# Performance work log

Measured on AMD Instinct MI355X. Metric: run time of the kernel, lower is better.

## Reference

```python
import jax, jax.numpy as jnp
import numpy as np

B = 4096          # batch_size
D_EMB = 16        # per-side embedding dim (embed_to_from width = 2*D_EMB)
D_HIGH = 784      # flattened high-dim feature size
NSR = 5           # negative_sample_rate
A = 1.576943      # UMAP _a
B_PARAM = 0.8950608  # UMAP _b
REPULSION = 1.0
EPS = 1e-4
GLOBAL_LOSS = 0.5
TOTAL_STEPS = 1000
BATCH_COUNT = 500  # fixed step for deterministic alpha/beta
WARMUP = int(0.05 * TOTAL_STEPS)


def _safe_sqrt(sq):
    # sqrt with zero (not NaN) gradient at 0, matching zero-distance pairs
    safe = jnp.where(sq > 0, sq, 1.0)
    return jnp.where(sq > 0, jnp.sqrt(safe), 0.0)


def _pairwise_dist(x):
    # ||x_i - x_j|| via gram trick; avoids materializing [N,N,D]
    sq = jnp.sum(x * x, axis=1)                      # [N]
    gram = x @ x.T                                   # [N,N]
    d2 = sq[:, None] + sq[None, :] - 2.0 * gram
    return _safe_sqrt(jnp.maximum(d2, 0.0))


def _umap_ce_loss(embed_to_from, perm):
    e_to, e_from = jnp.split(embed_to_from, 2, axis=1)   # [B, D_EMB] each
    neg_to = jnp.repeat(e_to, NSR, axis=0)               # [B*NSR, D_EMB]
    repeat_neg = jnp.repeat(e_from, NSR, axis=0)
    neg_from = repeat_neg[perm]                          # shuffled negatives
    d_pos = _safe_sqrt(jnp.sum((e_to - e_from) ** 2, axis=1))
    d_neg = _safe_sqrt(jnp.sum((neg_to - neg_from) ** 2, axis=1))
    dist = jnp.concatenate([d_pos, d_neg], axis=0)       # [B*(1+NSR)]
    p_dist = 1.0 / (1.0 + A * dist ** (2.0 * B_PARAM))
    p_graph = jnp.concatenate([jnp.ones(B, p_dist.dtype), jnp.zeros(B * NSR, p_dist.dtype)])
    attraction = -p_graph * jnp.log(jnp.clip(p_dist, EPS, 1.0))
    repellant = -(1.0 - p_graph) * jnp.log(jnp.clip(1.0 - p_dist, EPS, 1.0)) * REPULSION
    return jnp.mean(attraction + repellant)


def _global_feature_loss(embed_to_from, to_x):
    e_to = embed_to_from[:, :D_EMB]
    to_x = to_x.reshape(to_x.shape[0], -1)
    high_dis = _pairwise_dist(to_x)     # [N,N]
    low_dis = _pairwise_dist(e_to)      # [N,N]
    # row-wise pearson correlation between high_dis and low_dis
    h = high_dis - jnp.mean(high_dis, axis=1, keepdims=True)
    l = low_dis - jnp.mean(low_dis, axis=1, keepdims=True)
    num = jnp.sum(h * l, axis=1)
    den = jnp.sqrt(jnp.sum(h * h, axis=1)) * jnp.sqrt(jnp.sum(l * l, axis=1))
    corr = jnp.mean(num / den)
    return -corr


def _alpha_beta():
    if BATCH_COUNT >= WARMUP:
        if BATCH_COUNT <= 0.9 * TOTAL_STEPS:
            beta = max(0.0, GLOBAL_LOSS * (1 - BATCH_COUNT / (TOTAL_STEPS - WARMUP * 4)) ** 2)
        else:
            beta = 0.0
        alpha = max(0.0, 1 - beta)
    else:
        alpha = 0.0
        beta = GLOBAL_LOSS
    return alpha, beta


def setup_inputs() -> dict:
    key = jax.random.key(0)
    k1, k2, k3 = jax.random.split(key, 3)
    embed_to_from = jax.random.normal(k1, (B, 2 * D_EMB), dtype=jnp.float32)
    placeholder = jax.random.normal(k2, (B, D_HIGH), dtype=jnp.float32)
    perm = jax.random.permutation(k3, B * NSR).astype(jnp.int32)
    return {"embed_to_from": embed_to_from, "placeholder": placeholder, "perm": perm}


def reference(embed_to_from, placeholder, perm):
    loss = _umap_ce_loss(embed_to_from, perm)
    loss_g = _global_feature_loss(embed_to_from, placeholder)
    alpha, beta = _alpha_beta()
    return alpha * loss + beta * loss_g
```

## Files before the change

### kernel.cpp

```cpp
#include <hip/hip_runtime.h>
#include <hip/hip_bf16.h>
#include <math.h>

#define NB    4096
#define DH    784
#define NSR   5
#define NNEG  (NB*NSR)
#define NTOT  (NB + NNEG)

#define A_CONST 1.576943f
#define PEXP    1.7901216f
#define EPS_C   1.0e-4f
#define ALPHA_C 0.9296875f
#define BETA_C  0.0703125f

#define NBLK  528
#define CH    262144
#define SBUF  32768

typedef __hip_bfloat16 bf16;
typedef short bf16x8 __attribute__((ext_vector_type(8)));
typedef float f32x4  __attribute__((ext_vector_type(4)));
typedef float f32x2  __attribute__((ext_vector_type(2)));
typedef long long2v __attribute__((ext_vector_type(2)));

#define WS_XF8    0
#define WS_EBF    3407872
#define WS_SQX    3670016
#define WS_SQE    3686400
#define WS_ACC5   3702784
#define WS_UPART  8945664
#define WS_CNT    8946304

__device__ __forceinline__ void gl2lds16(const void* g, void* l) {
    __builtin_amdgcn_global_load_lds(
        (const __attribute__((address_space(1))) unsigned int*)g,
        (__attribute__((address_space(3))) unsigned int*)l,
        16, 0, 0);
}

__global__ void prep_fused(const float* __restrict__ X, const float* __restrict__ emb,
                           const int* __restrict__ perm, unsigned char* __restrict__ Xf8,
                           float* __restrict__ sqx, bf16* __restrict__ Ebf,
                           float* __restrict__ sqe, float* __restrict__ upart,
                           float* __restrict__ acc5, unsigned* __restrict__ cnt) {
    if (blockIdx.x == 0 && threadIdx.x == 0) *cnt = 0u;
    if (blockIdx.x < 1024) {
        const int wave = threadIdx.x >> 6, lane = threadIdx.x & 63;
        const int row = blockIdx.x * 4 + wave;
        const float4* xr = (const float4*)(X + (size_t)row * DH);
        int* xb = (int*)Xf8;
        float s = 0.f;
        #pragma unroll
        for (int it = 0; it < 4; ++it) {
            const int idx = lane + it * 64;
            if (idx < 208) {
                const int c = idx >> 4, p = idx & 15;
                const int q = p >> 2, h = (p >> 1) & 1, w = p & 1;
                const int src = c * 16 + h * 8 + q * 2 + w;
                int pk = 0;
                if (src < 196) {
                    float4 v = xr[src];
                    s += v.x * v.x + v.y * v.y + v.z * v.z + v.w * v.w;
                    int lo = __builtin_amdgcn_cvt_pk_fp8_f32(v.x, v.y, 0, false);
                    pk = __builtin_amdgcn_cvt_pk_fp8_f32(v.z, v.w, lo, true);
                }
                xb[(size_t)c * 65536 + (size_t)row * 16 + p] = pk;
            }
        }
        #pragma unroll
        for (int off = 32; off; off >>= 1) s += __shfl_down(s, off, 64);
        if (lane == 0) sqx[row] = s;
        return;
    }
    const int ub = blockIdx.x - 1024;
    const int t = ub * 256 + threadIdx.x;
    if (t < 5 * NB) acc5[t] = 0.f;
    float val = 0.f;
    if (t < NB) {
        const float4* av = (const float4*)(emb + (size_t)t * 32);
        float4 t0 = av[0], t1 = av[1], t2 = av[2], t3 = av[3];
        float4 f0 = av[4], f1 = av[5], f2 = av[6], f3 = av[7];
        bf16* eb = Ebf + (size_t)t * 32;
        union { bf16 h[4]; ushort4 u; } cv;
        #define ST4(dst, q) cv.h[0]=__float2bfloat16(q.x); cv.h[1]=__float2bfloat16(q.y); \
                            cv.h[2]=__float2bfloat16(q.z); cv.h[3]=__float2bfloat16(q.w); \
                            *(ushort4*)(dst) = cv.u;
        ST4(eb,      t0) ST4(eb + 4,  t1) ST4(eb + 8,  t2) ST4(eb + 12, t3)
        #undef ST4
        ushort4 z = {0, 0, 0, 0};
        *(ushort4*)(eb + 16) = z; *(ushort4*)(eb + 20) = z;
        *(ushort4*)(eb + 24) = z; *(ushort4*)(eb + 28) = z;
        sqe[t] = t0.x*t0.x + t0.y*t0.y + t0.z*t0.z + t0.w*t0.w
               + t1.x*t1.x + t1.y*t1.y + t1.z*t1.z + t1.w*t1.w
               + t2.x*t2.x + t2.y*t2.y + t2.z*t2.z + t2.w*t2.w
               + t3.x*t3.x + t3.y*t3.y + t3.z*t3.z + t3.w*t3.w;
        float d2 = 0.f;
        #define D2(a, b) { float4 df = {a.x-b.x, a.y-b.y, a.z-b.z, a.w-b.w}; \
                           d2 += df.x*df.x + df.y*df.y + df.z*df.z + df.w*df.w; }
        D2(t0, f0) D2(t1, f1) D2(t2, f2) D2(t3, f3)
        #undef D2
        float d = sqrtf(d2);
        float p = 1.f / (1.f + A_CONST * powf(d, PEXP));
        val = -logf(fminf(fmaxf(p, EPS_C), 1.f));
    } else if (t < NTOT) {
        const int k = t - NB;
        const int ti = k / 5;
        const int fi = perm[k] / 5;
        const float4* at = (const float4*)(emb + (size_t)ti * 32);
        const float4* bt = (const float4*)(emb + (size_t)fi * 32 + 16);
        float d2 = 0.f;
        #pragma unroll
        for (int q = 0; q < 4; ++q) {
            float4 a = at[q], b = bt[q];
            float4 df = {a.x-b.x, a.y-b.y, a.z-b.z, a.w-b.w};
            d2 += df.x*df.x + df.y*df.y + df.z*df.z + df.w*df.w;
        }
        float d = sqrtf(d2);
        float p = 1.f / (1.f + A_CONST * powf(d, PEXP));
        val = -logf(fminf(fmaxf(1.f - p, EPS_C), 1.f));
    }
    #pragma unroll
    for (int off = 32; off; off >>= 1) val += __shfl_down(val, off, 64);
    __shared__ float ps[4];
    if ((threadIdx.x & 63) == 0) ps[threadIdx.x >> 6] = val;
    __syncthreads();
    if (threadIdx.x == 0) upart[ub] = ps[0] + ps[1] + ps[2] + ps[3];
}

__global__ __launch_bounds__(512, 4) void gram_kernel(
    const unsigned char* __restrict__ Xf8, const bf16* __restrict__ Ebf,
    const float* __restrict__ sqx, const float* __restrict__ sqe,
    float* __restrict__ acc5, const float* __restrict__ upart,
    unsigned* __restrict__ cnt, float* __restrict__ out) {
    __shared__ __align__(16) unsigned char smem[67584];
    float* sqxs = (float*)(smem + 65536);
    float* sqes = (float*)(smem + 66560);
    float* scr  = (float*)smem;

    int bi, bj;
    {
        const int k = blockIdx.x & 7;
        const int idx = blockIdx.x >> 3;
        int g = -1, r = 0;
        if (k < 6) {
            const int SG[6] = {0,0,0,1,1,2}, SH[6] = {1,2,3,2,3,3};
            if (idx < 64) { bi = SG[k]*8 + (idx>>3); bj = SH[k]*8 + (idx&7); }
            else {
                const int DG[6] = {1,0,3,1,3,3};
                const int DR[6] = {32,34,30,34,32,34};
                g = DG[k]; r = DR[k] + (idx - 64);
            }
        } else if (k == 6) {
            if (idx < 34) { g = 0; r = idx; } else { g = 1; r = idx - 34; }
        } else {
            if (idx < 36) { g = 2; r = idx; } else { g = 3; r = idx - 36; }
        }
        if (g >= 0) {
            int a = 0;
            while (r >= 8 - a) { r -= 8 - a; ++a; }
            bi = g * 8 + a; bj = g * 8 + a + r;
        }
    }
    const int i0 = bi * 128, j0 = bj * 128;

    const int tid  = threadIdx.x;
    const int wave = tid >> 6;
    const int lane = tid & 63;
    const int wy = wave >> 1, wx = wave & 1;
    const int quad = lane >> 4, l15 = lane & 15;

    f32x4 acc[2][4];
    #pragma unroll
    for (int a = 0; a < 2; ++a)
        #pragma unroll
        for (int b = 0; b < 4; ++b)
            acc[a][b] = (f32x4){0.f, 0.f, 0.f, 0.f};

    const int rA  = lane >> 2;
    const int gsb = (((lane & 3) ^ ((lane >> 3) & 3))) * 16;
    const unsigned char* gA = Xf8 + (size_t)(i0 + wave * 16 + rA) * 64 + gsb;
    const unsigned char* gB = Xf8 + (size_t)(j0 + wave * 16 + rA) * 64 + gsb;
    const unsigned char* eA = (const unsigned char*)Ebf + (size_t)(i0 + wave * 16 + rA) * 64 + gsb;
    const unsigned char* eB = (const unsigned char*)Ebf + (size_t)(j0 + wave * 16 + rA) * 64 + gsb;

    if (tid < 128) {
        sqxs[tid] = sqx[i0 + tid]; sqxs[128 + tid] = sqx[j0 + tid];
        sqes[tid] = sqe[i0 + tid]; sqes[128 + tid] = sqe[j0 + tid];
    }
    __syncthreads();

#define STAGE_X(b, s) { \
        unsigned char* d = smem + (b) * SBUF + wave * 1024; \
        gl2lds16(gA + (size_t)(2 * (s)) * CH,     d); \
        gl2lds16(gA + (size_t)(2 * (s) + 1) * CH, d + 8192); \
        gl2lds16(gB + (size_t)(2 * (s)) * CH,     d + 16384); \
        gl2lds16(gB + (size_t)(2 * (s) + 1) * CH, d + 24576); }
#define STAGE_LAST(b) { \
        unsigned char* d = smem + (b) * SBUF + wave * 1024; \
        gl2lds16(gA + (size_t)12 * CH, d); \
        gl2lds16(eA,                   d + 8192); \
        gl2lds16(gB + (size_t)12 * CH, d + 16384); \
        gl2lds16(eB,                   d + 24576); }
#define MMX(aF, bF) { \
        _Pragma("unroll") \
        for (int mi = 0; mi < 2; ++mi) { \
            _Pragma("unroll") \
            for (int ni = 0; ni < 4; ++ni) { \
                acc[mi][ni] = __builtin_amdgcn_mfma_f32_16x16x32_fp8_fp8( \
                    aF[mi][0], bF[ni][0], acc[mi][ni], 0, 0, 0); \
                acc[mi][ni] = __builtin_amdgcn_mfma_f32_16x16x32_fp8_fp8( \
                    aF[mi][1], bF[ni][1], acc[mi][ni], 0, 0, 0); \
            } \
        } }

    STAGE_X(0, 0)
    STAGE_X(1, 1)

    const int key = (l15 >> 1) & 3;
    const int boX = ((quad ^ key) << 4);
    const int aro = (wy * 32 + l15) * 64 + boX;
    const int bro = (wx * 64 + l15) * 64 + boX;

    #pragma unroll
    for (int t = 0; t < 7; ++t) {
        if (t < 6) { asm volatile("s_waitcnt vmcnt(4)" ::: "memory"); }
        else       { asm volatile("s_waitcnt vmcnt(0)" ::: "memory"); }
        __builtin_amdgcn_s_barrier();
        const unsigned char* bb = smem + (t & 1) * SBUF;
        long2v aF0[2], bF0[4];
        #pragma unroll
        for (int mi = 0; mi < 2; ++mi)
            aF0[mi] = *(const long2v*)&bb[aro + mi * 1024];
        #pragma unroll
        for (int ni = 0; ni < 4; ++ni)
            bF0[ni] = *(const long2v*)&bb[16384 + bro + ni * 1024];
        __builtin_amdgcn_s_setprio(1);
        MMX(aF0, bF0)
        __builtin_amdgcn_s_setprio(0);
        if (t < 6) {
            long2v aF1[2], bF1[4];
            #pragma unroll
            for (int mi = 0; mi < 2; ++mi)
                aF1[mi] = *(const long2v*)&bb[8192 + aro + mi * 1024];
            #pragma unroll
            for (int ni = 0; ni < 4; ++ni)
                bF1[ni] = *(const long2v*)&bb[24576 + bro + ni * 1024];
            if (t < 5) {
                asm volatile("s_waitcnt lgkmcnt(0)" ::: "memory");
                __builtin_amdgcn_sched_barrier(0);
                __builtin_amdgcn_s_barrier();
                if (t < 4) { STAGE_X(t & 1, t + 2) }
                else       { STAGE_LAST(0) }
            }
            __builtin_amdgcn_s_setprio(1);
            MMX(aF1, bF1)
            __builtin_amdgcn_s_setprio(0);
        }
    }
#undef STAGE_X
#undef STAGE_LAST
#undef MMX

    bf16x8 afE[2], bfrE[4];
    #pragma unroll
    for (int mi = 0; mi < 2; ++mi)
        afE[mi] = *(const bf16x8*)&smem[8192 + aro + mi * 1024];
    #pragma unroll
    for (int ni = 0; ni < 4; ++ni)
        bfrE[ni] = *(const bf16x8*)&smem[24576 + bro + ni * 1024];
    float sqxj[4], sqej[4];
    #pragma unroll
    for (int ni = 0; ni < 4; ++ni) {
        const int jl = wx * 64 + ni * 16 + l15;
        sqxj[ni] = sqxs[128 + jl]; sqej[ni] = sqes[128 + jl];
    }
    __syncthreads();

    float cst[4][5];
    #pragma unroll
    for (int ni = 0; ni < 4; ++ni)
        #pragma unroll
        for (int c = 0; c < 5; ++c) cst[ni][c] = 0.f;

    #pragma unroll
    for (int mi = 0; mi < 2; ++mi) {
        f32x4 aE[4];
        #pragma unroll
        for (int ni = 0; ni < 4; ++ni) {
            f32x4 z = (f32x4){0.f, 0.f, 0.f, 0.f};
            aE[ni] = __builtin_amdgcn_mfma_f32_16x16x32_bf16(afE[mi], bfrE[ni], z, 0, 0, 0);
        }
        const int ilb = wy * 32 + mi * 16 + quad * 4;
        float sqxi[4], sqei[4];
        #pragma unroll
        for (int r = 0; r < 4; ++r) { sqxi[r] = sqxs[ilb + r]; sqei[r] = sqes[ilb + r]; }
        float rs[5][4];
        #pragma unroll
        for (int c = 0; c < 5; ++c)
            #pragma unroll
            for (int r = 0; r < 4; ++r) rs[c][r] = 0.f;
        #pragma unroll
        for (int ni = 0; ni < 4; ++ni) {
            const int j = j0 + wx * 64 + ni * 16 + l15;
            #pragma unroll
            for (int r = 0; r < 4; ++r) {
                const int i = i0 + ilb + r;
                float H, L;
                if (i == j) { H = 0.f; L = 0.f; }
                else {
                    float d2  = sqxi[r] + sqxj[ni] - 2.0f * acc[mi][ni][r];
                    H = sqrtf(fmaxf(d2, 0.f));
                    float d2e = sqei[r] + sqej[ni] - 2.0f * aE[ni][r];
                    L = sqrtf(fmaxf(d2e, 0.f));
                }
                rs[0][r] += H; rs[1][r] += H * H; rs[2][r] += L;
                rs[3][r] += L * L; rs[4][r] += H * L;
                cst[ni][0] += H; cst[ni][1] += H * H; cst[ni][2] += L;
                cst[ni][3] += L * L; cst[ni][4] += H * L;
            }
        }
        #pragma unroll
        for (int c = 0; c < 5; ++c)
            #pragma unroll
            for (int r = 0; r < 4; ++r)
                scr[(size_t)((((wx * 5 + c) << 6) + (wy << 4) + (quad << 2) + r)) * 18 + l15]
                    = rs[c][r];
        __syncthreads();
        for (int o = tid; o < 320; o += 512) {
            const int c = o >> 6, li = o & 63;
            const float* p0 = scr + (size_t)((c << 6) + li) * 18;
            const float* p1 = scr + (size_t)(((5 + c) << 6) + li) * 18;
            float s = 0.f;
            #pragma unroll
            for (int k = 0; k < 16; k += 2) {
                f32x2 v0 = *(const f32x2*)&p0[k]; s += v0.x + v0.y;
                f32x2 v1 = *(const f32x2*)&p1[k]; s += v1.x + v1.y;
            }
            const int iloc = ((li >> 4) << 5) + mi * 16 + (li & 15);
            unsafeAtomicAdd(&acc5[(size_t)c * NB + (i0 + iloc)], s);
        }
        __syncthreads();
    }

    if (bi != bj) {
        #pragma unroll
        for (int ni = 0; ni < 4; ++ni) {
            const int jl = wx * 64 + ni * 16 + l15;
            #pragma unroll
            for (int c = 0; c < 5; ++c)
                scr[(size_t)(c * 128 + jl) * 17 + (wy << 2) + quad] = cst[ni][c];
        }
        __syncthreads();
        for (int o = tid; o < 640; o += 512) {
            const int c = o >> 7, j = o & 127;
            const float* p = scr + (size_t)(c * 128 + j) * 17;
            float s = (((p[0] + p[1]) + (p[2] + p[3])) + ((p[4] + p[5]) + (p[6] + p[7])))
                    + (((p[8] + p[9]) + (p[10] + p[11])) + ((p[12] + p[13]) + (p[14] + p[15])));
            unsafeAtomicAdd(&acc5[(size_t)c * NB + (j0 + j)], s);
        }
    }

    __shared__ int lastFlag;
    __syncthreads();
    if (tid == 0) {
        __threadfence();
        lastFlag = (atomicAdd(cnt, 1u) == (unsigned)(NBLK - 1));
    }
    __syncthreads();
    if (lastFlag) {
        __threadfence();
        const float invN = 1.0f / (float)NB;
        float v = 0.f;
        #pragma unroll
        for (int rr = 0; rr < 8; ++rr) {
            const int r = tid + rr * 512;
            const float a  = acc5[0 * NB + r];
            const float b  = acc5[1 * NB + r];
            const float c2 = acc5[2 * NB + r];
            const float d  = acc5[3 * NB + r];
            const float e  = acc5[4 * NB + r];
            float num = e - a * c2 * invN;
            float vh  = fmaxf(b - a * a * invN, 0.f);
            float vl  = fmaxf(d - c2 * c2 * invN, 0.f);
            v += num / (sqrtf(vh) * sqrtf(vl));
        }
        v *= (-BETA_C * invN);
        if (tid < 96) v += upart[tid] * (ALPHA_C / (float)NTOT);
        #pragma unroll
        for (int off = 32; off; off >>= 1) v += __shfl_down(v, off, 64);
        float* fin = (float*)smem;
        __syncthreads();
        if ((tid & 63) == 0) fin[tid >> 6] = v;
        __syncthreads();
        if (tid == 0)
            out[0] = ((fin[0] + fin[1]) + (fin[2] + fin[3]))
                   + ((fin[4] + fin[5]) + (fin[6] + fin[7]));
    }
}

extern "C" void kernel_launch(void* const* d_in, const int* in_sizes, int n_in,
                              void* d_out, int out_size, void* d_ws, size_t ws_size,
                              hipStream_t stream) {
    const float* emb  = (const float*)d_in[0];
    const float* ph   = (const float*)d_in[1];
    const int*   perm = (const int*)d_in[2];
    float* out = (float*)d_out;

    char* ws = (char*)d_ws;
    unsigned char* Xf8 = (unsigned char*)(ws + WS_XF8);
    bf16*  Ebf    = (bf16*) (ws + WS_EBF);
    float* sqx    = (float*)(ws + WS_SQX);
    float* sqe    = (float*)(ws + WS_SQE);
    float* acc5   = (float*)(ws + WS_ACC5);
    float* upart  = (float*)(ws + WS_UPART);
    unsigned* cnt = (unsigned*)(ws + WS_CNT);

    prep_fused<<<1120, 256, 0, stream>>>(ph, emb, perm, Xf8, sqx, Ebf, sqe, upart, acc5, cnt);
    gram_kernel<<<NBLK, 512, 0, stream>>>(Xf8, Ebf, sqx, sqe, acc5, upart, cnt, out);
}
```

Baseline: 107.7 us.

## Compute two column tiles per block to reuse A-tile loads in gram kernel

After: 122.1 us. +13.4%, slower.

```diff
diff --git a/kernel.cpp b/kernel.cpp
--- a/kernel.cpp
+++ b/kernel.cpp
@@ -14,9 +14,9 @@
 #define ALPHA_C 0.9296875f
 #define BETA_C  0.0703125f
 
-#define NBLK  528
+#define NBLK  272
 #define CH    262144
-#define SBUF  32768
+#define SBUF  24576
 
 typedef __hip_bfloat16 bf16;
 typedef short bf16x8 __attribute__((ext_vector_type(8)));
@@ -128,41 +128,24 @@
     if (threadIdx.x == 0) upart[ub] = ps[0] + ps[1] + ps[2] + ps[3];
 }
 
-__global__ __launch_bounds__(512, 4) void gram_kernel(
+__global__ __launch_bounds__(512) void gram_kernel(
     const unsigned char* __restrict__ Xf8, const bf16* __restrict__ Ebf,
     const float* __restrict__ sqx, const float* __restrict__ sqe,
     float* __restrict__ acc5, const float* __restrict__ upart,
     unsigned* __restrict__ cnt, float* __restrict__ out) {
-    __shared__ __align__(16) unsigned char smem[67584];
-    float* sqxs = (float*)(smem + 65536);
-    float* sqes = (float*)(smem + 66560);
-    float* scr  = (float*)smem;
-
-    int bi, bj;
-    {
-        const int k = blockIdx.x & 7;
-        const int idx = blockIdx.x >> 3;
-        int g = -1, r = 0;
-        if (k < 6) {
-            const int SG[6] = {0,0,0,1,1,2}, SH[6] = {1,2,3,2,3,3};
-            if (idx < 64) { bi = SG[k]*8 + (idx>>3); bj = SH[k]*8 + (idx&7); }
-            else {
-                const int DG[6] = {1,0,3,1,3,3};
-                const int DR[6] = {32,34,30,34,32,34};
-                g = DG[k]; r = DR[k] + (idx - 64);
-            }
-        } else if (k == 6) {
-            if (idx < 34) { g = 0; r = idx; } else { g = 1; r = idx - 34; }
-        } else {
-            if (idx < 36) { g = 2; r = idx; } else { g = 3; r = idx - 36; }
-        }
-        if (g >= 0) {
-            int a = 0;
-            while (r >= 8 - a) { r -= 8 - a; ++a; }
-            bi = g * 8 + a; bj = g * 8 + a + r;
-        }
-    }
-    const int i0 = bi * 128, j0 = bj * 128;
+    __shared__ __align__(16) unsigned char smem[52224];
+    float* sqxs  = (float*)(smem + 49152);
+    float* sqes  = (float*)(smem + 49664);
+    float* sqxsj = (float*)(smem + 50176);
+    float* sqesj = (float*)(smem + 51200);
+    float* scr   = (float*)smem;
+
+    int n = (blockIdx.x & 7) * 34 + (blockIdx.x >> 3);
+    int bi = 0;
+    while (n >= ((33 - bi) >> 1)) { n -= (33 - bi) >> 1; ++bi; }
+    const int bj = bi + 2 * n;
+    const int has2 = (bj < 31);
+    const int i0 = bi * 128, j0s = bj * 128;
 
     const int tid  = threadIdx.x;
     const int wave = tid >> 6;
@@ -170,47 +153,38 @@
     const int wy = wave >> 1, wx = wave & 1;
     const int quad = lane >> 4, l15 = lane & 15;
 
-    f32x4 acc[2][4];
-    #pragma unroll
-    for (int a = 0; a < 2; ++a)
-        #pragma unroll
-        for (int b = 0; b < 4; ++b)
-            acc[a][b] = (f32x4){0.f, 0.f, 0.f, 0.f};
+    f32x4 acc[2][2][4];
+    #pragma unroll
+    for (int cc = 0; cc < 2; ++cc)
+        #pragma unroll
+        for (int a = 0; a < 2; ++a)
+            #pragma unroll
+            for (int b = 0; b < 4; ++b)
+                acc[cc][a][b] = (f32x4){0.f, 0.f, 0.f, 0.f};
 
     const int rA  = lane >> 2;
     const int gsb = (((lane & 3) ^ ((lane >> 3) & 3))) * 16;
-    const unsigned char* gA = Xf8 + (size_t)(i0 + wave * 16 + rA) * 64 + gsb;
-    const unsigned char* gB = Xf8 + (size_t)(j0 + wave * 16 + rA) * 64 + gsb;
-    const unsigned char* eA = (const unsigned char*)Ebf + (size_t)(i0 + wave * 16 + rA) * 64 + gsb;
-    const unsigned char* eB = (const unsigned char*)Ebf + (size_t)(j0 + wave * 16 + rA) * 64 + gsb;
-
-    if (tid < 128) {
-        sqxs[tid] = sqx[i0 + tid]; sqxs[128 + tid] = sqx[j0 + tid];
-        sqes[tid] = sqe[i0 + tid]; sqes[128 + tid] = sqe[j0 + tid];
-    }
+    const unsigned char* gA  = Xf8 + (size_t)(i0 + wave * 16 + rA) * 64 + gsb;
+    const unsigned char* gB0 = Xf8 + (size_t)(j0s + wave * 32 + rA) * 64 + gsb;
+
+    if (tid < 128) { sqxs[tid] = sqx[i0 + tid]; sqes[tid] = sqe[i0 + tid]; }
+    if (tid < 256) { sqxsj[tid] = sqx[j0s + tid]; sqesj[tid] = sqe[j0s + tid]; }
     __syncthreads();
 
 #define STAGE_X(b, s) { \
-        unsigned char* d = smem + (b) * SBUF + wave * 1024; \
-        gl2lds16(gA + (size_t)(2 * (s)) * CH,     d); \
-        gl2lds16(gA + (size_t)(2 * (s) + 1) * CH, d + 8192); \
-        gl2lds16(gB + (size_t)(2 * (s)) * CH,     d + 16384); \
-        gl2lds16(gB + (size_t)(2 * (s) + 1) * CH, d + 24576); }
-#define STAGE_LAST(b) { \
-        unsigned char* d = smem + (b) * SBUF + wave * 1024; \
-        gl2lds16(gA + (size_t)12 * CH, d); \
-        gl2lds16(eA,                   d + 8192); \
-        gl2lds16(gB + (size_t)12 * CH, d + 16384); \
-        gl2lds16(eB,                   d + 24576); }
-#define MMX(aF, bF) { \
+        unsigned char* d = smem + (b) * SBUF; \
+        gl2lds16(gA  + (size_t)(s) * CH, d + wave * 1024); \
+        gl2lds16(gB0 + (size_t)(s) * CH, d + 8192 + wave * 2048); \
+        gl2lds16(gB0 + (size_t)(s) * CH + 1024, d + 8192 + wave * 2048 + 1024); }
+#define MMX(ac, aF, bF) { \
         _Pragma("unroll") \
         for (int mi = 0; mi < 2; ++mi) { \
             _Pragma("unroll") \
             for (int ni = 0; ni < 4; ++ni) { \
-                acc[mi][ni] = __builtin_amdgcn_mfma_f32_16x16x32_fp8_fp8( \
-                    aF[mi][0], bF[ni][0], acc[mi][ni], 0, 0, 0); \
-                acc[mi][ni] = __builtin_amdgcn_mfma_f32_16x16x32_fp8_fp8( \
-                    aF[mi][1], bF[ni][1], acc[mi][ni], 0, 0, 0); \
+                ac[mi][ni] = __builtin_amdgcn_mfma_f32_16x16x32_fp8_fp8( \
+                    aF[mi][0], bF[ni][0], ac[mi][ni], 0, 0, 0); \
+                ac[mi][ni] = __builtin_amdgcn_mfma_f32_16x16x32_fp8_fp8( \
+                    aF[mi][1], bF[ni][1], ac[mi][ni], 0, 0, 0); \
             } \
         } }
 
@@ -223,141 +197,139 @@
     const int bro = (wx * 64 + l15) * 64 + boX;
 
     #pragma unroll
-    for (int t = 0; t < 7; ++t) {
-        if (t < 6) { asm volatile("s_waitcnt vmcnt(4)" ::: "memory"); }
-        else       { asm volatile("s_waitcnt vmcnt(0)" ::: "memory"); }
+    for (int t = 0; t < 13; ++t) {
+        if (t < 12) { asm volatile("s_waitcnt vmcnt(3)" ::: "memory"); }
+        else        { asm volatile("s_waitcnt vmcnt(0)" ::: "memory"); }
         __builtin_amdgcn_s_barrier();
         const unsigned char* bb = smem + (t & 1) * SBUF;
-        long2v aF0[2], bF0[4];
+        long2v aF[2], bF0[4], bF1[4];
         #pragma unroll
         for (int mi = 0; mi < 2; ++mi)
-            aF0[mi] = *(const long2v*)&bb[aro + mi * 1024];
+            aF[mi] = *(const long2v*)&bb[aro + mi * 1024];
         #pragma unroll
         for (int ni = 0; ni < 4; ++ni)
-            bF0[ni] = *(const long2v*)&bb[16384 + bro + ni * 1024];
-        __builtin_amdgcn_s_setprio(1);
-        MMX(aF0, bF0)
-        __builtin_amdgcn_s_setprio(0);
-        if (t < 6) {
-            long2v aF1[2], bF1[4];
-            #pragma unroll
-            for (int mi = 0; mi < 2; ++mi)
-                aF1[mi] = *(const long2v*)&bb[8192 + aro + mi * 1024];
-            #pragma unroll
-            for (int ni = 0; ni < 4; ++ni)
-                bF1[ni] = *(const long2v*)&bb[24576 + bro + ni * 1024];
-            if (t < 5) {
-                asm volatile("s_waitcnt lgkmcnt(0)" ::: "memory");
-                __builtin_amdgcn_sched_barrier(0);
-                __builtin_amdgcn_s_barrier();
-                if (t < 4) { STAGE_X(t & 1, t + 2) }
-                else       { STAGE_LAST(0) }
-            }
-            __builtin_amdgcn_s_setprio(1);
-            MMX(aF1, bF1)
-            __builtin_amdgcn_s_setprio(0);
-        }
+            bF0[ni] = *(const long2v*)&bb[8192 + bro + ni * 1024];
+        #pragma unroll
+        for (int ni = 0; ni < 4; ++ni)
+            bF1[ni] = *(const long2v*)&bb[16384 + bro + ni * 1024];
+        if (t < 11) {
+            asm volatile("s_waitcnt lgkmcnt(0)" ::: "memory");
+            __builtin_amdgcn_sched_barrier(0);
+            __builtin_amdgcn_s_barrier();
+            STAGE_X(t & 1, t + 2)
+        }
+        MMX(acc[0], aF, bF0)
+        MMX(acc[1], aF, bF1)
     }
 #undef STAGE_X
-#undef STAGE_LAST
 #undef MMX
 
-    bf16x8 afE[2], bfrE[4];
+    __syncthreads();
+
+    const unsigned char* Eb = (const unsigned char*)Ebf;
+    bf16x8 afE[2];
     #pragma unroll
     for (int mi = 0; mi < 2; ++mi)
-        afE[mi] = *(const bf16x8*)&smem[8192 + aro + mi * 1024];
-    #pragma unroll
-    for (int ni = 0; ni < 4; ++ni)
-        bfrE[ni] = *(const bf16x8*)&smem[24576 + bro + ni * 1024];
-    float sqxj[4], sqej[4];
-    #pragma unroll
-    for (int ni = 0; ni < 4; ++ni) {
-        const int jl = wx * 64 + ni * 16 + l15;
-        sqxj[ni] = sqxs[128 + jl]; sqej[ni] = sqes[128 + jl];
-    }
-    __syncthreads();
-
-    float cst[4][5];
-    #pragma unroll
-    for (int ni = 0; ni < 4; ++ni)
-        #pragma unroll
-        for (int c = 0; c < 5; ++c) cst[ni][c] = 0.f;
-
-    #pragma unroll
-    for (int mi = 0; mi < 2; ++mi) {
-        f32x4 aE[4];
+        afE[mi] = *(const bf16x8*)(Eb + (size_t)(i0 + wy * 32 + mi * 16 + l15) * 64 + quad * 16);
+
+    #pragma unroll
+    for (int cc = 0; cc < 2; ++cc) {
+        if (cc == 1 && !has2) continue;
+        const int bjc = bj + cc;
+        const int j0 = bjc * 128;
+        bf16x8 bfrE[4];
+        #pragma unroll
+        for (int ni = 0; ni < 4; ++ni)
+            bfrE[ni] = *(const bf16x8*)(Eb + (size_t)(j0 + wx * 64 + ni * 16 + l15) * 64 + quad * 16);
+        float sqxj[4], sqej[4];
         #pragma unroll
         for (int ni = 0; ni < 4; ++ni) {
-            f32x4 z = (f32x4){0.f, 0.f, 0.f, 0.f};
-            aE[ni] = __builtin_amdgcn_mfma_f32_16x16x32_bf16(afE[mi], bfrE[ni], z, 0, 0, 0);
-        }
-        const int ilb = wy * 32 + mi * 16 + quad * 4;
-        float sqxi[4], sqei[4];
-        #pragma unroll
-        for (int r = 0; r < 4; ++r) { sqxi[r] = sqxs[ilb + r]; sqei[r] = sqes[ilb + r]; }
-        float rs[5][4];
-        #pragma unroll
-        for (int c = 0; c < 5; ++c)
-            #pragma unroll
-            for (int r = 0; r < 4; ++r) rs[c][r] = 0.f;
-        #pragma unroll
-        for (int ni = 0; ni < 4; ++ni) {
-            const int j = j0 + wx * 64 + ni * 16 + l15;
-            #pragma unroll
-            for (int r = 0; r < 4; ++r) {
-                const int i = i0 + ilb + r;
-                float H, L;
-                if (i == j) { H = 0.f; L = 0.f; }
-                else {
-                    float d2  = sqxi[r] + sqxj[ni] - 2.0f * acc[mi][ni][r];
-                    H = sqrtf(fmaxf(d2, 0.f));
-                    float d2e = sqei[r] + sqej[ni] - 2.0f * aE[ni][r];
-                    L = sqrtf(fmaxf(d2e, 0.f));
+            const int jl = cc * 128 + wx * 64 + ni * 16 + l15;
+            sqxj[ni] = sqxsj[jl]; sqej[ni] = sqesj[jl];
+        }
+        float cst[4][5];
+        #pragma unroll
+        for (int ni = 0; ni < 4; ++ni)
+            #pragma unroll
+            for (int c = 0; c < 5; ++c) cst[ni][c] = 0.f;
+
+        #pragma unroll
+        for (int mi = 0; mi < 2; ++mi) {
+            f32x4 aE[4];
+            #pragma unroll
+            for (int ni = 0; ni < 4; ++ni) {
+                f32x4 z = (f32x4){0.f, 0.f, 0.f, 0.f};
+                aE[ni] = __builtin_amdgcn_mfma_f32_16x16x32_bf16(afE[mi], bfrE[ni], z, 0, 0, 0);
+            }
+            const int ilb = wy * 32 + mi * 16 + quad * 4;
+            float sqxi[4], sqei[4];
+            #pragma unroll
+            for (int r = 0; r < 4; ++r) { sqxi[r] = sqxs[ilb + r]; sqei[r] = sqes[ilb + r]; }
+            float rs[5][4];
+            #pragma unroll
+            for (int c = 0; c < 5; ++c)
+                #pragma unroll
+                for (int r = 0; r < 4; ++r) rs[c][r] = 0.f;
+            #pragma unroll
+            for (int ni = 0; ni < 4; ++ni) {
+                const int j = j0 + wx * 64 + ni * 16 + l15;
+                #pragma unroll
+                for (int r = 0; r < 4; ++r) {
+                    const int i = i0 + ilb + r;
+                    float H, L;
+                    if (i == j) { H = 0.f; L = 0.f; }
+                    else {
+                        float d2  = sqxi[r] + sqxj[ni] - 2.0f * acc[cc][mi][ni][r];
+                        H = sqrtf(fmaxf(d2, 0.f));
+                        float d2e = sqei[r] + sqej[ni] - 2.0f * aE[ni][r];
+                        L = sqrtf(fmaxf(d2e, 0.f));
+                    }
+                    rs[0][r] += H; rs[1][r] += H * H; rs[2][r] += L;
+                    rs[3][r] += L * L; rs[4][r] += H * L;
+                    cst[ni][0] += H; cst[ni][1] += H * H; cst[ni][2] += L;
+                    cst[ni][3] += L * L; cst[ni][4] += H * L;
                 }
-                rs[0][r] += H; rs[1][r] += H * H; rs[2][r] += L;
-                rs[3][r] += L * L; rs[4][r] += H * L;
-                cst[ni][0] += H; cst[ni][1] += H * H; cst[ni][2] += L;
-                cst[ni][3] += L * L; cst[ni][4] += H * L;
-            }
-        }
-        #pragma unroll
-        for (int c = 0; c < 5; ++c)
-            #pragma unroll
-            for (int r = 0; r < 4; ++r)
-                scr[(size_t)((((wx * 5 + c) << 6) + (wy << 4) + (quad << 2) + r)) * 18 + l15]
-                    = rs[c][r];
-        __syncthreads();
-        for (int o = tid; o < 320; o += 512) {
-            const int c = o >> 6, li = o & 63;
-            const float* p0 = scr + (size_t)((c << 6) + li) * 18;
-            const float* p1 = scr + (size_t)(((5 + c) << 6) + li) * 18;
-            float s = 0.f;
-            #pragma unroll
-            for (int k = 0; k < 16; k += 2) {
-                f32x2 v0 = *(const f32x2*)&p0[k]; s += v0.x + v0.y;
-                f32x2 v1 = *(const f32x2*)&p1[k]; s += v1.x + v1.y;
-            }
-            const int iloc = ((li >> 4) << 5) + mi * 16 + (li & 15);
-            unsafeAtomicAdd(&acc5[(size_t)c * NB + (i0 + iloc)], s);
-        }
-        __syncthreads();
-    }
-
-    if (bi != bj) {
-        #pragma unroll
-        for (int ni = 0; ni < 4; ++ni) {
-            const int jl = wx * 64 + ni * 16 + l15;
+            }
             #pragma unroll
             for (int c = 0; c < 5; ++c)
-                scr[(size_t)(c * 128 + jl) * 17 + (wy << 2) + quad] = cst[ni][c];
-        }
-        __syncthreads();
-        for (int o = tid; o < 640; o += 512) {
-            const int c = o >> 7, j = o & 127;
-            const float* p = scr + (size_t)(c * 128 + j) * 17;
-            float s = (((p[0] + p[1]) + (p[2] + p[3])) + ((p[4] + p[5]) + (p[6] + p[7])))
-                    + (((p[8] + p[9]) + (p[10] + p[11])) + ((p[12] + p[13]) + (p[14] + p[15])));
-            unsafeAtomicAdd(&acc5[(size_t)c * NB + (j0 + j)], s);
+                #pragma unroll
+                for (int r = 0; r < 4; ++r)
+                    scr[(size_t)((((wx * 5 + c) << 6) + (wy << 4) + (quad << 2) + r)) * 18 + l15]
+                        = rs[c][r];
+            __syncthreads();
+            for (int o = tid; o < 320; o += 512) {
+                const int c = o >> 6, li = o & 63;
+                const float* p0 = scr + (size_t)((c << 6) + li) * 18;
+                const float* p1 = scr + (size_t)(((5 + c) << 6) + li) * 18;
+                float s = 0.f;
+                #pragma unroll
+                for (int k = 0; k < 16; k += 2) {
+                    f32x2 v0 = *(const f32x2*)&p0[k]; s += v0.x + v0.y;
+                    f32x2 v1 = *(const f32x2*)&p1[k]; s += v1.x + v1.y;
+                }
+                const int iloc = ((li >> 4) << 5) + mi * 16 + (li & 15);
+                unsafeAtomicAdd(&acc5[(size_t)c * NB + (i0 + iloc)], s);
+            }
+            __syncthreads();
+        }
+
+        if (bi != bjc) {
+            #pragma unroll
+            for (int ni = 0; ni < 4; ++ni) {
+                const int jl = wx * 64 + ni * 16 + l15;
+                #pragma unroll
+                for (int c = 0; c < 5; ++c)
+                    scr[(size_t)(c * 128 + jl) * 17 + (wy << 2) + quad] = cst[ni][c];
+            }
+            __syncthreads();
+            for (int o = tid; o < 640; o += 512) {
+                const int c = o >> 7, j = o & 127;
+                const float* p = scr + (size_t)(c * 128 + j) * 17;
+                float s = (((p[0] + p[1]) + (p[2] + p[3])) + ((p[4] + p[5]) + (p[6] + p[7])))
+                        + (((p[8] + p[9]) + (p[10] + p[11])) + ((p[12] + p[13]) + (p[14] + p[15])));
+                unsafeAtomicAdd(&acc5[(size_t)c * NB + (j0 + j)], s);
+            }
+            __syncthreads();
         }
     }
 
```
